# Kernel tuning notes

Measured on AMD Instinct MI355X. Metric: run time of the kernel, lower is better.

## Reference

```python
import jax, jax.numpy as jnp
import numpy as np

N_NODES = 100000
N_EDGES = 3200000
N_GRAPHS = 256
HID = 32
IN_DIM = 6
BN_EPS = 1e-5


def setup_inputs() -> dict:
    key = jax.random.key(0)
    ks = jax.random.split(key, 24)
    inp = {}
    inp['x'] = jax.random.normal(ks[0], (N_NODES, IN_DIM), dtype=jnp.float32)
    inp['edge_index'] = jax.random.randint(ks[1], (2, N_EDGES), 0, N_NODES)
    inp['pos'] = jax.random.normal(ks[2], (N_NODES, 6), dtype=jnp.float32)
    inp['batch'] = jnp.sort(jax.random.randint(ks[3], (N_NODES,), 0, N_GRAPHS))
    # GaussKernel params
    inp['inv_sigma1'] = jax.random.uniform(ks[4], (1,)) * 0.02 + 0.99
    inp['inv_sigma2'] = jax.random.uniform(ks[5], (1,)) * 0.02 + 0.99
    # GCNConv weights (glorot-ish scale) + biases
    dims = [IN_DIM, HID, HID, HID, HID]
    for i in range(4):
        s = 1.0 / np.sqrt(dims[i])
        inp[f'W{i+1}'] = jax.random.normal(ks[6 + i], (dims[i], dims[i + 1]), dtype=jnp.float32) * s
        inp[f'b{i+1}'] = jnp.zeros((dims[i + 1],), dtype=jnp.float32)
    # BatchNorm (layers 1..3 only; last layer has no BN) - eval mode params
    for i in range(3):
        inp[f'g{i+1}'] = jnp.ones((HID,), dtype=jnp.float32)
        inp[f'be{i+1}'] = jnp.zeros((HID,), dtype=jnp.float32)
    # post-MP linear HID -> 1
    inp['Wout'] = jax.random.normal(ks[20], (HID, 1), dtype=jnp.float32) * (1.0 / np.sqrt(HID))
    inp['bout'] = jnp.zeros((1,), dtype=jnp.float32)
    return inp


def _gauss_kernel(pos, row, col, s1, s2):
    p1, p2 = pos[row, :3], pos[col, :3]
    a1, a2 = pos[row, 3:], pos[col, 3:]
    D = jnp.sum((p1 - p2) ** 2, axis=-1)               # [E]
    T = (1.0 - jnp.sum(a1 * a2, axis=-1)) ** 2         # [E]
    return jnp.exp(-(D * s1[0] ** 2 + T * s2[0] ** 2))  # [E]


def _gcn_conv(x, W, b, row, col, ew):
    # PyG GCNConv (normalize=True, add_self_loops=True, fill_value=1.0)
    n = x.shape[0]
    xw = x @ W                                          # [N, out]
    deg = jnp.zeros((n,), xw.dtype).at[col].add(ew) + 1.0  # self-loop weight 1
    dinv = jnp.where(deg > 0, deg ** -0.5, 0.0)
    norm = dinv[row] * ew * dinv[col]                   # [E]
    out = jnp.zeros_like(xw).at[col].add(norm[:, None] * xw[row])
    out = out + (dinv * dinv)[:, None] * xw             # self-loop messages
    return out + b


def _bn_eval(x, g, be):
    # running_mean=0, running_var=1 at init (inference mode)
    return x * (g / jnp.sqrt(1.0 + BN_EPS)) + be


def reference(x, edge_index, pos, batch, inv_sigma1, inv_sigma2,
              W1, b1, W2, b2, W3, b3, W4, b4,
              g1, be1, g2, be2, g3, be3, Wout, bout):
    row, col = edge_index[0], edge_index[1]
    ew = _gauss_kernel(pos, row, col, inv_sigma1, inv_sigma2)
    # layer 1..3: GCN -> BN -> ReLU (dropout is identity in eval)
    h = x
    for (W, b, g, be) in ((W1, b1, g1, be1), (W2, b2, g2, be2), (W3, b3, g3, be3)):
        h = _gcn_conv(h, W, b, row, col, ew)
        h = jax.nn.relu(_bn_eval(h, g, be))
    # layer 4: plain GCN (no BN / act / dropout)
    h = _gcn_conv(h, W4, b4, row, col, ew)
    emb = h
    # graph task: global mean pool then Linear + Sigmoid
    sums = jax.ops.segment_sum(h, batch, num_segments=N_GRAPHS)
    cnts = jax.ops.segment_sum(jnp.ones((h.shape[0],), h.dtype), batch, num_segments=N_GRAPHS)
    pooled = sums / jnp.maximum(cnts, 1.0)[:, None]
    pred = jax.nn.sigmoid(pooled @ Wout + bout)
    return (emb, pred)
```

## Files before the change

### kernel.cpp

```cpp
#include <hip/hip_runtime.h>
#include <hip/hip_bf16.h>
#include <math.h>

#define TB 256
#define TB_BIN 512
#define NBLK 256
#define PCHUNK 1024
#define SLOTS 72
#define NPB 64
#define MAXNB 2048

__device__ __forceinline__ void atomic_add_f32(float* p, float v) {
    unsafeAtomicAdd(p, v);
}

__device__ __forceinline__ unsigned short f2bf(float x) {
    unsigned u = __float_as_uint(x);
    return (unsigned short)((u + 0x7FFF + ((u >> 16) & 1)) >> 16);
}
__device__ __forceinline__ float4 bf4(ushort4 u) {
    return make_float4(__uint_as_float((unsigned)u.x << 16),
                       __uint_as_float((unsigned)u.y << 16),
                       __uint_as_float((unsigned)u.z << 16),
                       __uint_as_float((unsigned)u.w << 16));
}

__global__ __launch_bounds__(TB) void zero_pack_kernel(float* __restrict__ sums,
                                                       float* __restrict__ cnt,
                                                       const float2* __restrict__ pos2,
                                                       float4* __restrict__ pos8,
                                                       int n_nodes) {
    int i = blockIdx.x * TB + threadIdx.x;
    if (i < n_nodes) {
        float2 a = pos2[i * 3 + 0], b = pos2[i * 3 + 1], c = pos2[i * 3 + 2];
        pos8[i * 2 + 0] = make_float4(a.x, a.y, b.x, b.y);
        pos8[i * 2 + 1] = make_float4(c.x, c.y, 0.f, 0.f);
    }
    if (i < 256 * 32) sums[i] = 0.0f;
    if (i < 256) cnt[i] = 0.0f;
}

__global__ __launch_bounds__(TB_BIN) void count_kernel(
    const int* __restrict__ col, int* __restrict__ blkcnt,
    int nb, int n_edges, int chunk) {
    __shared__ int h[MAXNB];
    int blk = blockIdx.x, tid = threadIdx.x;
    for (int i = tid; i < nb; i += TB_BIN) h[i] = 0;
    __syncthreads();
    size_t s = (size_t)blk * chunk;
    size_t e1 = min(s + (size_t)chunk, (size_t)n_edges);
    for (size_t e = s + tid; e < e1; e += TB_BIN) {
        int c = __builtin_nontemporal_load(&col[e]);
        atomicAdd(&h[c >> 6], 1);
    }
    __syncthreads();
    for (int i = tid; i < nb; i += TB_BIN) blkcnt[(size_t)blk * nb + i] = h[i];
}

__global__ __launch_bounds__(TB) void scanA_kernel(
    const int* __restrict__ blkcnt, int* __restrict__ blkpre,
    int* __restrict__ cnt, int nb) {
    int b = blockIdx.x * TB + threadIdx.x;
    if (b >= nb) return;
    int run = 0;
#pragma unroll 4
    for (int blk = 0; blk < NBLK; blk++) {
        size_t idx = (size_t)blk * nb + b;
        int v = blkcnt[idx];
        blkpre[idx] = run;
        run += v;
    }
    cnt[b] = run;
}

__global__ __launch_bounds__(TB) void scanB_kernel(
    const int* __restrict__ cnt, int* __restrict__ off, int nb) {
    __shared__ int part[TB];
    int t = threadIdx.x;
    int chunk = (nb + TB - 1) / TB;
    int s0 = t * chunk, s1 = min(s0 + chunk, nb);
    int s = 0;
    for (int i = s0; i < s1; i++) s += cnt[i];
    part[t] = s;
    __syncthreads();
    for (int d = 1; d < TB; d <<= 1) {
        int v = (t >= d) ? part[t - d] : 0;
        __syncthreads();
        part[t] += v;
        __syncthreads();
    }
    int run = (t == 0) ? 0 : part[t - 1];
    for (int i = s0; i < s1; i++) { off[i] = run; run += cnt[i]; }
    if (t == TB - 1) off[nb] = part[TB - 1];
}

__global__ __launch_bounds__(TB_BIN) void scatter_kernel(
    const int* __restrict__ row, const int* __restrict__ col,
    const int* __restrict__ blkpre, const int* __restrict__ off,
    unsigned* __restrict__ records, int nb, int n_edges, int chunk) {
    __shared__ int base[MAXNB];
    __shared__ int cur[MAXNB];
    int blk = blockIdx.x, tid = threadIdx.x;
    for (int i = tid; i < nb; i += TB_BIN) {
        base[i] = off[i] + blkpre[(size_t)blk * nb + i];
        cur[i] = 0;
    }
    __syncthreads();
    size_t s = (size_t)blk * chunk;
    size_t e1 = min(s + (size_t)chunk, (size_t)n_edges);
    for (size_t e = s + tid; e < e1; e += TB_BIN) {
        int r = __builtin_nontemporal_load(&row[e]);
        int c = __builtin_nontemporal_load(&col[e]);
        int bk = c >> 6;
        int lr = atomicAdd(&cur[bk], 1);
        unsigned rec = (unsigned)r | ((unsigned)(c & (NPB - 1)) << 17);
        records[(size_t)base[bk] + lr] = rec;
    }
}

__global__ __launch_bounds__(TB) void build_kernel(
    const unsigned* __restrict__ records, const int* __restrict__ off,
    const float4* __restrict__ pos8,
    const float* __restrict__ s1p, const float* __restrict__ s2p,
    int* __restrict__ hist, float* __restrict__ dinv,
    int2* __restrict__ csr, int n_nodes) {
    __shared__ float4 cpos[NPB * 2];
    __shared__ int lhist[NPB];
    __shared__ float lwsum[NPB];
    int b = blockIdx.x, tid = threadIdx.x;
    int cbase = b << 6;
    if (tid < NPB) { lhist[tid] = 0; lwsum[tid] = 0.0f; }
    if (tid < NPB * 2) {
        int node = cbase + (tid >> 1);
        if (node < n_nodes) cpos[tid] = pos8[(size_t)node * 2 + (tid & 1)];
    }
    __syncthreads();
    float s1 = s1p[0], s2 = s2p[0];
    int rs = off[b], re = off[b + 1];
    for (int e = rs + tid; e < re; e += TB) {
        unsigned rec = __builtin_nontemporal_load(&records[e]);
        int r = (int)(rec & 0x1FFFFu);
        int cl = (int)((rec >> 17) & (NPB - 1));
        float4 ra = pos8[(size_t)r * 2 + 0], rb = pos8[(size_t)r * 2 + 1];
        float4 ca = cpos[cl * 2 + 0], cb = cpos[cl * 2 + 1];
        float dx = ra.x - ca.x, dy = ra.y - ca.y, dz = ra.z - ca.z;
        float D = dx * dx + dy * dy + dz * dz;
        float dot = ra.w * ca.w + rb.x * cb.x + rb.y * cb.y;
        float t = 1.0f - dot;
        float w = expf(-(D * s1 * s1 + t * t * s2 * s2));
        int rank = atomicAdd(&lhist[cl], 1);
        atomicAdd(&lwsum[cl], w);
        if (rank < SLOTS)
            csr[(size_t)(cbase + cl) * SLOTS + rank] = make_int2(r, __float_as_int(w));
    }
    __syncthreads();
    if (tid < NPB) {
        int c = cbase + tid;
        if (c < n_nodes) {
            int cnt = min(lhist[tid], SLOTS);
            hist[c] = cnt;
            dinv[c] = rsqrtf(lwsum[tid] + 1.0f);
            int nseg = (cnt + 7) >> 3;
            size_t base = (size_t)c * SLOTS;
            for (int j = cnt; j < nseg * 8; j++) csr[base + j] = make_int2(0, 0);
        }
    }
}

template <int K, bool BN>
__global__ __launch_bounds__(TB) void matmul_kernel(
    const float* __restrict__ fin, const float* __restrict__ W,
    const float* __restrict__ g, const float* __restrict__ be,
    const float* __restrict__ dinv, unsigned short* __restrict__ ywb,
    int n_nodes) {
    __shared__ float Ws[K * 32];
    __shared__ float gs[32];
    __shared__ float bs[32];
    int tid = threadIdx.x;
    for (int i = tid; i < K * 32; i += TB) Ws[i] = W[i];
    if (BN && tid < 32) {
        gs[tid] = g[tid] * (1.0f / sqrtf(1.0f + 1e-5f));
        bs[tid] = be[tid];
    }
    __syncthreads();
    int n = blockIdx.x * TB + tid;
    if (n >= n_nodes) return;
    float vals[K];
    const float* fp = fin + (size_t)n * K;
    if (K % 4 == 0) {
#pragma unroll
        for (int k = 0; k < K / 4; k++) {
            float4 v = ((const float4*)fp)[k];
            vals[k * 4 + 0] = v.x;
            vals[k * 4 + 1] = v.y;
            vals[k * 4 + 2] = v.z;
            vals[k * 4 + 3] = v.w;
        }
    } else {
#pragma unroll
        for (int k = 0; k < K; k++) vals[k] = fp[k];
    }
    if (BN) {
#pragma unroll
        for (int k = 0; k < K; k++) vals[k] = fmaxf(fmaf(vals[k], gs[k], bs[k]), 0.0f);
    }
    float acc[32];
#pragma unroll
    for (int j = 0; j < 32; j++) acc[j] = 0.0f;
#pragma unroll
    for (int k = 0; k < K; k++) {
        float v = vals[k];
#pragma unroll
        for (int j = 0; j < 32; j++) acc[j] = fmaf(v, Ws[k * 32 + j], acc[j]);
    }
    float di = dinv[n];
    uint4* op = (uint4*)(ywb + (size_t)n * 32);
#pragma unroll
    for (int j = 0; j < 4; j++) {
        uint4 pk;
        pk.x = (unsigned)f2bf(di * acc[j * 8 + 0]) | ((unsigned)f2bf(di * acc[j * 8 + 1]) << 16);
        pk.y = (unsigned)f2bf(di * acc[j * 8 + 2]) | ((unsigned)f2bf(di * acc[j * 8 + 3]) << 16);
        pk.z = (unsigned)f2bf(di * acc[j * 8 + 4]) | ((unsigned)f2bf(di * acc[j * 8 + 5]) << 16);
        pk.w = (unsigned)f2bf(di * acc[j * 8 + 6]) | ((unsigned)f2bf(di * acc[j * 8 + 7]) << 16);
        op[j] = pk;
    }
}

__device__ __forceinline__ float4 f4_fma(float w, float4 v, float4 a) {
    return make_float4(fmaf(w, v.x, a.x), fmaf(w, v.y, a.y),
                       fmaf(w, v.z, a.z), fmaf(w, v.w, a.w));
}

__device__ __forceinline__ float4 gather_core(
    const int* __restrict__ hist, const int2* __restrict__ csr,
    const unsigned short* __restrict__ ywb, int n, int lane) {
    int o = lane >> 3, f4i = (lane & 7) * 4;
    int nseg = (min(hist[n], SLOTS) + 7) >> 3;
    size_t base = (size_t)n * SLOTS;
    float4 acc = make_float4(0.f, 0.f, 0.f, 0.f);
    for (int seg = o; seg < nseg; seg += 4) {
        const int4* q = (const int4*)(csr + base + (size_t)seg * 8);
        int4 q0 = q[0], q1 = q[1], q2 = q[2], q3 = q[3];
        ushort4 u0 = *(const ushort4*)(ywb + ((size_t)q0.x << 5) + f4i);
        ushort4 u1 = *(const ushort4*)(ywb + ((size_t)q0.z << 5) + f4i);
        ushort4 u2 = *(const ushort4*)(ywb + ((size_t)q1.x << 5) + f4i);
        ushort4 u3 = *(const ushort4*)(ywb + ((size_t)q1.z << 5) + f4i);
        ushort4 u4 = *(const ushort4*)(ywb + ((size_t)q2.x << 5) + f4i);
        ushort4 u5 = *(const ushort4*)(ywb + ((size_t)q2.z << 5) + f4i);
        ushort4 u6 = *(const ushort4*)(ywb + ((size_t)q3.x << 5) + f4i);
        ushort4 u7 = *(const ushort4*)(ywb + ((size_t)q3.z << 5) + f4i);
        acc = f4_fma(__int_as_float(q0.y), bf4(u0), acc);
        acc = f4_fma(__int_as_float(q0.w), bf4(u1), acc);
        acc = f4_fma(__int_as_float(q1.y), bf4(u2), acc);
        acc = f4_fma(__int_as_float(q1.w), bf4(u3), acc);
        acc = f4_fma(__int_as_float(q2.y), bf4(u4), acc);
        acc = f4_fma(__int_as_float(q2.w), bf4(u5), acc);
        acc = f4_fma(__int_as_float(q3.y), bf4(u6), acc);
        acc = f4_fma(__int_as_float(q3.w), bf4(u7), acc);
    }
    float4 t;
    t.x = __shfl_xor(acc.x, 8, 32); t.y = __shfl_xor(acc.y, 8, 32);
    t.z = __shfl_xor(acc.z, 8, 32); t.w = __shfl_xor(acc.w, 8, 32);
    acc.x += t.x; acc.y += t.y; acc.z += t.z; acc.w += t.w;
    t.x = __shfl_xor(acc.x, 16, 32); t.y = __shfl_xor(acc.y, 16, 32);
    t.z = __shfl_xor(acc.z, 16, 32); t.w = __shfl_xor(acc.w, 16, 32);
    acc.x += t.x; acc.y += t.y; acc.z += t.z; acc.w += t.w;
    return acc;
}

__global__ __launch_bounds__(TB) void fused_layer_kernel(
    const int* __restrict__ hist, const int2* __restrict__ csr,
    const unsigned short* __restrict__ ywb_in, const float* __restrict__ dinv,
    const float4* __restrict__ bias4, const float* __restrict__ g,
    const float* __restrict__ be, const float* __restrict__ W,
    unsigned short* __restrict__ ywb_out, int n_nodes) {
    __shared__ float Ws[32 * 32];
    __shared__ float gs[32];
    __shared__ float bs[32];
    int tid = threadIdx.x;
    for (int i = tid; i < 32 * 32; i += TB) Ws[i] = W[i];
    if (tid < 32) {
        gs[tid] = g[tid] * (1.0f / sqrtf(1.0f + 1e-5f));
        bs[tid] = be[tid];
    }
    __syncthreads();
    int n = blockIdx.x * (TB / 32) + (tid >> 5);
    if (n >= n_nodes) return;
    int lane = tid & 31, f4i = (lane & 7) * 4;
    float4 acc = gather_core(hist, csr, ywb_in, n, lane);
    float di = dinv[n];
    ushort4 us = *(const ushort4*)(ywb_in + ((size_t)n << 5) + f4i);
    float4 self = bf4(us);
    float4 bb = bias4[f4i >> 2];
    float4 h;
    h.x = fmaf(di, acc.x + self.x, bb.x);
    h.y = fmaf(di, acc.y + self.y, bb.y);
    h.z = fmaf(di, acc.z + self.z, bb.z);
    h.w = fmaf(di, acc.w + self.w, bb.w);
    h.x = fmaxf(fmaf(h.x, gs[f4i + 0], bs[f4i + 0]), 0.0f);
    h.y = fmaxf(fmaf(h.y, gs[f4i + 1], bs[f4i + 1]), 0.0f);
    h.z = fmaxf(fmaf(h.z, gs[f4i + 2], bs[f4i + 2]), 0.0f);
    h.w = fmaxf(fmaf(h.w, gs[f4i + 3], bs[f4i + 3]), 0.0f);
    float y = 0.0f;
#pragma unroll
    for (int q = 0; q < 8; q++) {
        float hx = __shfl(h.x, q, 32);
        float hy = __shfl(h.y, q, 32);
        float hz = __shfl(h.z, q, 32);
        float hw = __shfl(h.w, q, 32);
        y = fmaf(hx, Ws[(4 * q + 0) * 32 + lane], y);
        y = fmaf(hy, Ws[(4 * q + 1) * 32 + lane], y);
        y = fmaf(hz, Ws[(4 * q + 2) * 32 + lane], y);
        y = fmaf(hw, Ws[(4 * q + 3) * 32 + lane], y);
    }
    ywb_out[(size_t)n * 32 + lane] = f2bf(di * y);
}

__global__ __launch_bounds__(TB) void gather_node_kernel(
    const int* __restrict__ hist, const int2* __restrict__ csr,
    const unsigned short* __restrict__ ywb, const float* __restrict__ dinv,
    const float4* __restrict__ bias4, float* __restrict__ agg, int n_nodes) {
    int n = blockIdx.x * (TB / 32) + (threadIdx.x >> 5);
    if (n >= n_nodes) return;
    int lane = threadIdx.x & 31;
    int o = lane >> 3, f4i = (lane & 7) * 4;
    float4 acc = gather_core(hist, csr, ywb, n, lane);
    if (o == 0) {
        float di = dinv[n];
        ushort4 us = *(const ushort4*)(ywb + ((size_t)n << 5) + f4i);
        float4 self = bf4(us);
        float4 bb = bias4[f4i >> 2];
        float4 v;
        v.x = fmaf(di, acc.x + self.x, bb.x);
        v.y = fmaf(di, acc.y + self.y, bb.y);
        v.z = fmaf(di, acc.z + self.z, bb.z);
        v.w = fmaf(di, acc.w + self.w, bb.w);
        ((float4*)agg)[(size_t)n * 8 + (f4i >> 2)] = v;
    }
}

__global__ __launch_bounds__(TB) void pool_kernel(
    const float* __restrict__ agg, const int* __restrict__ batch,
    float* __restrict__ sums, float* __restrict__ cnt, int n_nodes) {
    int j = threadIdx.x & 31;
    int s = threadIdx.x >> 5;
    int base = blockIdx.x * PCHUNK;
    int endn = min(base + PCHUNK, n_nodes);
    float acc = 0.0f;
    float cacc = 0.0f;
    int cur = -1;
    for (int n = base + s; n < endn; n += 8) {
        int bg = batch[n];
        float v = agg[(size_t)n * 32 + j];
        if (bg != cur) {
            if (cur >= 0) {
                atomic_add_f32(&sums[(size_t)cur * 32 + j], acc);
                if (j == 0) atomic_add_f32(&cnt[cur], cacc);
            }
            cur = bg; acc = 0.0f; cacc = 0.0f;
        }
        acc += v;
        cacc += 1.0f;
    }
    if (cur >= 0) {
        atomic_add_f32(&sums[(size_t)cur * 32 + j], acc);
        if (j == 0) atomic_add_f32(&cnt[cur], cacc);
    }
}

__global__ __launch_bounds__(TB) void pred_kernel(
    const float* __restrict__ sums, const float* __restrict__ cnt,
    const float* __restrict__ Wout, const float* __restrict__ bout,
    float* __restrict__ out) {
    int g = blockIdx.x * TB + threadIdx.x;
    if (g >= 256) return;
    float c = fmaxf(cnt[g], 1.0f);
    float acc = 0.0f;
#pragma unroll
    for (int j = 0; j < 32; j++) acc += sums[g * 32 + j] * Wout[j];
    float z = acc / c + bout[0];
    out[g] = 1.0f / (1.0f + expf(-z));
}

extern "C" void kernel_launch(void* const* d_in, const int* in_sizes, int n_in,
                              void* d_out, int out_size, void* d_ws, size_t ws_size,
                              hipStream_t stream) {
    const float* x = (const float*)d_in[0];
    const int* edge_index = (const int*)d_in[1];
    const float* pos = (const float*)d_in[2];
    const int* batch = (const int*)d_in[3];
    const float* s1 = (const float*)d_in[4];
    const float* s2 = (const float*)d_in[5];
    const float* W1 = (const float*)d_in[6];
    const float* b1 = (const float*)d_in[7];
    const float* W2 = (const float*)d_in[8];
    const float* b2 = (const float*)d_in[9];
    const float* W3 = (const float*)d_in[10];
    const float* b3 = (const float*)d_in[11];
    const float* W4 = (const float*)d_in[12];
    const float* b4 = (const float*)d_in[13];
    const float* g1 = (const float*)d_in[14];
    const float* be1 = (const float*)d_in[15];
    const float* g2 = (const float*)d_in[16];
    const float* be2 = (const float*)d_in[17];
    const float* g3 = (const float*)d_in[18];
    const float* be3 = (const float*)d_in[19];
    const float* Wout = (const float*)d_in[20];
    const float* bout = (const float*)d_in[21];

    const size_t E = (size_t)in_sizes[1] / 2;
    const size_t N = (size_t)in_sizes[3];

    const int* row = edge_index;
    const int* col = edge_index + E;

    const int NB = (int)((N + NPB - 1) / NPB);
    const int chunk = (int)((E + NBLK - 1) / NBLK);

    auto align256 = [](size_t v) { return (v + 255) & ~(size_t)255; };
    char* w = (char*)d_ws;
    int2* csr = (int2*)w;      w += align256(N * SLOTS * 8);
    int* hist = (int*)w;       w += align256(N * 4);
    unsigned short* ywbA = (unsigned short*)w; w += align256(N * 32 * 2);
    unsigned short* ywbB = (unsigned short*)w; w += align256(N * 32 * 2);
    float4* pos8 = (float4*)w; w += align256(N * 8 * 4);
    float* dinv = (float*)w;   w += align256(N * 4);
    float* sums = (float*)w;   w += align256(256 * 32 * 4);
    float* cnt = (float*)w;    w += align256(256 * 4);
    int* blkcnt = (int*)w;     w += align256((size_t)NBLK * NB * 4);
    int* blkpre = (int*)w;     w += align256((size_t)NBLK * NB * 4);
    int* bcnt = (int*)w;       w += align256((size_t)NB * 4);
    int* boff = (int*)w;       w += align256((size_t)(NB + 1) * 4);

    float* out_emb = (float*)d_out;
    float* out_pred = (float*)d_out + N * 32;

    unsigned* records = (unsigned*)d_out;

    const int gN = (int)((N + TB - 1) / TB);
    const int gW = (int)((N + (TB / 32) - 1) / (TB / 32));
    const int gP = (int)((N + PCHUNK - 1) / PCHUNK);
    const int gSA = (NB + TB - 1) / TB;

    zero_pack_kernel<<<gN, TB, 0, stream>>>(sums, cnt, (const float2*)pos,
                                            pos8, (int)N);
    count_kernel<<<NBLK, TB_BIN, 0, stream>>>(col, blkcnt, NB, (int)E, chunk);
    scanA_kernel<<<gSA, TB, 0, stream>>>(blkcnt, blkpre, bcnt, NB);
    scanB_kernel<<<1, TB, 0, stream>>>(bcnt, boff, NB);
    scatter_kernel<<<NBLK, TB_BIN, 0, stream>>>(row, col, blkpre, boff,
                                                records, NB, (int)E, chunk);
    build_kernel<<<NB, TB, 0, stream>>>(records, boff, pos8, s1, s2,
                                        hist, dinv, csr, (int)N);

    matmul_kernel<6, false><<<gN, TB, 0, stream>>>(x, W1, nullptr, nullptr, dinv,
                                                   ywbA, (int)N);
    fused_layer_kernel<<<gW, TB, 0, stream>>>(hist, csr, ywbA, dinv,
                                              (const float4*)b1, g1, be1, W2,
                                              ywbB, (int)N);
    fused_layer_kernel<<<gW, TB, 0, stream>>>(hist, csr, ywbB, dinv,
                                              (const float4*)b2, g2, be2, W3,
                                              ywbA, (int)N);
    fused_layer_kernel<<<gW, TB, 0, stream>>>(hist, csr, ywbA, dinv,
                                              (const float4*)b3, g3, be3, W4,
                                              ywbB, (int)N);
    gather_node_kernel<<<gW, TB, 0, stream>>>(hist, csr, ywbB, dinv,
                                              (const float4*)b4, out_emb, (int)N);

    pool_kernel<<<gP, TB, 0, stream>>>(out_emb, batch, sums, cnt, (int)N);
    pred_kernel<<<1, TB, 0, stream>>>(sums, cnt, Wout, bout, out_pred);
}
```

Baseline: 501.3 us.

## Compute Gauss edge weights in scatter pass and widen binning blocks

Moves the Gaussian edge-weight computation from build_kernel into scatter_kernel. There row and col positions are read in the original edge order, and the weight is written to a side array held in the ywbA buffer. build_kernel then only reads the packed records and weights, with no random pos gathers and no shared-memory staging of column positions. The binning block size doubles to 1024 threads, and count_kernel uses a normal load instead of a nontemporal one. In exchange there is an extra 4-byte-per-edge write and read, plus random pos8 gathers for both endpoints in scatter.

Result: slower. 605.0 us (+20.7%).

```diff
diff --git a/kernel.cpp b/kernel.cpp
--- a/kernel.cpp
+++ b/kernel.cpp
@@ -3,7 +3,7 @@
 #include <math.h>
 
 #define TB 256
-#define TB_BIN 512
+#define TB_BIN 1024
 #define NBLK 256
 #define PCHUNK 1024
 #define SLOTS 72
@@ -50,7 +50,7 @@
     size_t s = (size_t)blk * chunk;
     size_t e1 = min(s + (size_t)chunk, (size_t)n_edges);
     for (size_t e = s + tid; e < e1; e += TB_BIN) {
-        int c = __builtin_nontemporal_load(&col[e]);
+        int c = col[e];
         atomicAdd(&h[c >> 6], 1);
     }
     __syncthreads();
@@ -96,8 +96,11 @@
 
 __global__ __launch_bounds__(TB_BIN) void scatter_kernel(
     const int* __restrict__ row, const int* __restrict__ col,
+    const float4* __restrict__ pos8,
+    const float* __restrict__ s1p, const float* __restrict__ s2p,
     const int* __restrict__ blkpre, const int* __restrict__ off,
-    unsigned* __restrict__ records, int nb, int n_edges, int chunk) {
+    unsigned* __restrict__ rec4, float* __restrict__ warr,
+    int nb, int n_edges, int chunk) {
     __shared__ int base[MAXNB];
     __shared__ int cur[MAXNB];
     int blk = blockIdx.x, tid = threadIdx.x;
@@ -106,6 +109,7 @@
         cur[i] = 0;
     }
     __syncthreads();
+    float s1 = s1p[0], s2 = s2p[0];
     size_t s = (size_t)blk * chunk;
     size_t e1 = min(s + (size_t)chunk, (size_t)n_edges);
     for (size_t e = s + tid; e < e1; e += TB_BIN) {
@@ -113,41 +117,36 @@
         int c = __builtin_nontemporal_load(&col[e]);
         int bk = c >> 6;
         int lr = atomicAdd(&cur[bk], 1);
-        unsigned rec = (unsigned)r | ((unsigned)(c & (NPB - 1)) << 17);
-        records[(size_t)base[bk] + lr] = rec;
+        float4 ra = pos8[(size_t)r * 2 + 0], rb = pos8[(size_t)r * 2 + 1];
+        float4 ca = pos8[(size_t)c * 2 + 0], cb = pos8[(size_t)c * 2 + 1];
+        float dx = ra.x - ca.x, dy = ra.y - ca.y, dz = ra.z - ca.z;
+        float D = dx * dx + dy * dy + dz * dz;
+        float dot = ra.w * ca.w + rb.x * cb.x + rb.y * cb.y;
+        float t = 1.0f - dot;
+        float w = expf(-(D * s1 * s1 + t * t * s2 * s2));
+        size_t idx = (size_t)base[bk] + lr;
+        rec4[idx] = (unsigned)r | ((unsigned)(c & (NPB - 1)) << 17);
+        warr[idx] = w;
     }
 }
 
 __global__ __launch_bounds__(TB) void build_kernel(
-    const unsigned* __restrict__ records, const int* __restrict__ off,
-    const float4* __restrict__ pos8,
-    const float* __restrict__ s1p, const float* __restrict__ s2p,
+    const unsigned* __restrict__ rec4, const float* __restrict__ warr,
+    const int* __restrict__ off,
     int* __restrict__ hist, float* __restrict__ dinv,
     int2* __restrict__ csr, int n_nodes) {
-    __shared__ float4 cpos[NPB * 2];
     __shared__ int lhist[NPB];
     __shared__ float lwsum[NPB];
     int b = blockIdx.x, tid = threadIdx.x;
     int cbase = b << 6;
     if (tid < NPB) { lhist[tid] = 0; lwsum[tid] = 0.0f; }
-    if (tid < NPB * 2) {
-        int node = cbase + (tid >> 1);
-        if (node < n_nodes) cpos[tid] = pos8[(size_t)node * 2 + (tid & 1)];
-    }
-    __syncthreads();
-    float s1 = s1p[0], s2 = s2p[0];
+    __syncthreads();
     int rs = off[b], re = off[b + 1];
     for (int e = rs + tid; e < re; e += TB) {
-        unsigned rec = __builtin_nontemporal_load(&records[e]);
+        unsigned rec = __builtin_nontemporal_load(&rec4[e]);
+        float w = __builtin_nontemporal_load(&warr[e]);
         int r = (int)(rec & 0x1FFFFu);
         int cl = (int)((rec >> 17) & (NPB - 1));
-        float4 ra = pos8[(size_t)r * 2 + 0], rb = pos8[(size_t)r * 2 + 1];
-        float4 ca = cpos[cl * 2 + 0], cb = cpos[cl * 2 + 1];
-        float dx = ra.x - ca.x, dy = ra.y - ca.y, dz = ra.z - ca.z;
-        float D = dx * dx + dy * dy + dz * dz;
-        float dot = ra.w * ca.w + rb.x * cb.x + rb.y * cb.y;
-        float t = 1.0f - dot;
-        float w = expf(-(D * s1 * s1 + t * t * s2 * s2));
         int rank = atomicAdd(&lhist[cl], 1);
         atomicAdd(&lwsum[cl], w);
         if (rank < SLOTS)
@@ -435,7 +434,8 @@
     float* out_emb = (float*)d_out;
     float* out_pred = (float*)d_out + N * 32;
 
-    unsigned* records = (unsigned*)d_out;
+    unsigned* rec4 = (unsigned*)d_out;
+    float* warr = (float*)ywbA;
 
     const int gN = (int)((N + TB - 1) / TB);
     const int gW = (int)((N + (TB / 32) - 1) / (TB / 32));
@@ -447,10 +447,10 @@
     count_kernel<<<NBLK, TB_BIN, 0, stream>>>(col, blkcnt, NB, (int)E, chunk);
     scanA_kernel<<<gSA, TB, 0, stream>>>(blkcnt, blkpre, bcnt, NB);
     scanB_kernel<<<1, TB, 0, stream>>>(bcnt, boff, NB);
-    scatter_kernel<<<NBLK, TB_BIN, 0, stream>>>(row, col, blkpre, boff,
-                                                records, NB, (int)E, chunk);
-    build_kernel<<<NB, TB, 0, stream>>>(records, boff, pos8, s1, s2,
-                                        hist, dinv, csr, (int)N);
+    scatter_kernel<<<NBLK, TB_BIN, 0, stream>>>(row, col, pos8, s1, s2,
+                                                blkpre, boff, rec4, warr,
+                                                NB, (int)E, chunk);
+    build_kernel<<<NB, TB, 0, stream>>>(rec4, warr, boff, hist, dinv, csr, (int)N);
 
     matmul_kernel<6, false><<<gN, TB, 0, stream>>>(x, W1, nullptr, nullptr, dinv,
                                                    ywbA, (int)N);
```
